# Kernel tuning notes

Hardware: AMD Instinct MI355X
Metric: run time of the kernel (lower is better)

## Reference

```python
import jax, jax.numpy as jnp
import numpy as np

N_NODES = 100000
N_EDGES = 1600000
N_PAIRS = 500000
IN_C, HID_C, OUT_C = 128, 128, 128


def setup_inputs() -> dict:
    key = jax.random.key(0)
    ks = jax.random.split(key, 12)
    def lin(k, fan_in, shape):
        b = 1.0 / np.sqrt(fan_in)
        return jax.random.uniform(k, shape, jnp.float32, -b, b)
    return {
        "x": jax.random.normal(ks[0], (N_NODES, IN_C), jnp.float32),
        "edge_index": jax.random.randint(ks[1], (2, N_EDGES), 0, N_NODES),
        "edge_pairs": jax.random.randint(ks[2], (2, N_PAIRS), 0, N_NODES),
        "W1": lin(ks[3], IN_C, (IN_C, HID_C)),
        "b1": jnp.zeros((HID_C,), jnp.float32),
        "W2": lin(ks[4], HID_C, (HID_C, OUT_C)),
        "b2": jnp.zeros((OUT_C,), jnp.float32),
        "Wm1": lin(ks[5], 2 * OUT_C, (2 * OUT_C, HID_C)),
        "bm1": lin(ks[6], 2 * OUT_C, (HID_C,)),
        "Wm2": lin(ks[7], HID_C, (HID_C, 1)),
        "bm2": lin(ks[8], HID_C, (1,)),
    }


def reference(x, edge_index, edge_pairs, W1, b1, W2, b2, Wm1, bm1, Wm2, bm2):
    N = x.shape[0]
    loop = jnp.arange(N, dtype=edge_index.dtype)
    row = jnp.concatenate([edge_index[0], loop])  # source nodes (+self loops)
    col = jnp.concatenate([edge_index[1], loop])  # target nodes (+self loops)
    # symmetric GCN normalization: deg^{-1/2}[row] * deg^{-1/2}[col]
    deg = jax.ops.segment_sum(jnp.ones(col.shape, x.dtype), col, num_segments=N)
    dinv = jnp.where(deg > 0, jax.lax.rsqrt(deg), 0.0)
    norm = dinv[row] * dinv[col]  # [E+N]

    def gcn_conv(h, W, b):
        h = h @ W  # transform first (PyG GCNConv lin has no bias)
        msg = h[row] * norm[:, None]
        return jax.ops.segment_sum(msg, col, num_segments=N) + b

    h = jax.nn.relu(gcn_conv(x, W1, b1))
    h = gcn_conv(h, W2, b2)  # dropout p=0.0 -> identity

    src, dst = edge_pairs[0], edge_pairs[1]
    ef = jnp.concatenate([h[src], h[dst]], axis=-1)  # [P, 2*out]
    out = jax.nn.relu(ef @ Wm1 + bm1) @ Wm2 + bm2
    return out.squeeze(-1)
```

## Files before the change

kernel.cpp:

```cpp
#include <hip/hip_runtime.h>
#include <hip/hip_fp16.h>

#define NCH 128
#define G_NODES 256
#define EPB 4096
#define RCAP 4864
#define MAXNB 512
#define KST 40

typedef __attribute__((ext_vector_type(8))) short short8;
typedef _Float16 half8 __attribute__((ext_vector_type(8)));
typedef __attribute__((ext_vector_type(4))) float floatx4;

static inline size_t align256(size_t x){ return (x + 255) & ~(size_t)255; }

__global__ __launch_bounds__(256) void binA_kernel(
    const int* __restrict__ row, const int* __restrict__ col,
    int* __restrict__ gcur, unsigned* __restrict__ bucketed, int E, int NB,
    const float* __restrict__ W1, const float* __restrict__ W2,
    const float* __restrict__ Wm1, short* __restrict__ planes){
  __shared__ int cnt[MAXNB];
  __shared__ int lbase[MAXNB];
  __shared__ int gbase[MAXNB];
  __shared__ unsigned sorted[EPB];
  __shared__ unsigned short binOf[EPB];
  __shared__ int sh[256];
  __shared__ int carry;
  int t = threadIdx.x;
  int e0 = blockIdx.x * EPB;
  int ecnt = min(EPB, E - e0);
  for (int i = t; i < NB; i += 256) cnt[i] = 0;
  if (t == 0) carry = 0;
  __syncthreads();
  unsigned rec[16]; int bn[16]; int rk[16];
  #pragma unroll
  for (int i = 0; i < 16; i++){
    int e = e0 + i * 256 + t;
    if (e < E){
      int r = row[e], c = col[e];
      bn[i]  = c >> 8;
      rec[i] = (unsigned)r | ((unsigned)(c & 255) << 17);
      rk[i]  = atomicAdd(&cnt[bn[i]], 1);
    } else bn[i] = -1;
  }
  __syncthreads();
  for (int start = 0; start < NB; start += 256){
    int i = start + t;
    int v = (i < NB) ? cnt[i] : 0;
    sh[t] = v; __syncthreads();
    for (int off = 1; off < 256; off <<= 1){
      int val = (t >= off) ? sh[t - off] : 0;
      __syncthreads(); sh[t] += val; __syncthreads();
    }
    if (i < NB) lbase[i] = sh[t] - v + carry;
    __syncthreads();
    if (t == 255) carry += sh[255];
    __syncthreads();
  }
  for (int i = t; i < NB; i += 256){
    int c = cnt[i];
    gbase[i] = (c > 0) ? atomicAdd(&gcur[i], c) : 0;
  }
  __syncthreads();
  #pragma unroll
  for (int i = 0; i < 16; i++){
    if (bn[i] >= 0){
      int pos = lbase[bn[i]] + rk[i];
      sorted[pos] = rec[i];
      binOf[pos]  = (unsigned short)bn[i];
    }
  }
  __syncthreads();
  for (int idx = t; idx < ecnt; idx += 256){
    int b = binOf[idx];
    int gpos = gbase[b] + (idx - lbase[b]);
    if (gpos < RCAP) bucketed[(size_t)b * RCAP + gpos] = sorted[idx];
  }
  {
    int gid = blockIdx.x * 256 + t;
    if (gid < 4 * 16384){
      int mat = gid >> 14;
      int idx = gid & 16383;
      int k = idx >> 7, n = idx & 127;
      const float* src = (mat == 0) ? W1 : (mat == 1) ? W2 : (mat == 2) ? Wm1 : (Wm1 + 16384);
      float x = src[idx];
      short hs, ls;
      if (mat == 0){
        unsigned u = __float_as_uint(x);
        hs = (short)(u >> 16);
        float hf = __uint_as_float(u & 0xFFFF0000u);
        ls = (short)(__float_as_uint(x - hf) >> 16);
      } else {
        __half h = __float2half(x);
        __half l = __float2half(x - __half2float(h));
        hs = __half_as_short(h); ls = __half_as_short(l);
      }
      planes[(size_t)(2 * mat) * 16384 + n * 128 + k]     = hs;
      planes[(size_t)(2 * mat + 1) * 16384 + n * 128 + k] = ls;
    }
  }
}

__global__ __launch_bounds__(512, 4) void fused_gemm_binB(
    const float* __restrict__ X, const short* __restrict__ Whi_,
    const short* __restrict__ Wlo_, __half* __restrict__ O, int nrows, int gemmBlocks,
    const unsigned* __restrict__ bucketed, const int* __restrict__ gcur,
    int* __restrict__ rows_sorted, int* __restrict__ offs,
    int* __restrict__ counts, float* __restrict__ dinv, int N){
  __shared__ __align__(16) char smem[40960];
  int t = threadIdx.x;
  if (blockIdx.x < gemmBlocks){
    short* Xhi = (short*)smem;
    short* Xlo = Xhi + 128 * KST;
    short* Whi = Xlo + 128 * KST;
    short* Wlo = Whi + 128 * KST;
    int w = t >> 6, lane = t & 63;
    int m = lane & 15, q = lane >> 4;
    int row0 = blockIdx.x * 128;
    floatx4 acc[8];
    #pragma unroll
    for (int ct = 0; ct < 8; ct++) acc[ct] = (floatx4)0.f;
    for (int kc = 0; kc < 4; kc++){
      int k0 = kc * 32;
      __syncthreads();
      #pragma unroll
      for (int qq = 0; qq < 2; qq++){
        int f = t + 512 * qq;
        int r = f >> 3, kq = f & 7;
        int gr = row0 + r;
        int grc = (gr < nrows) ? gr : 0;
        float4 v = *(const float4*)(X + (size_t)grc * NCH + k0 + kq * 4);
        short h[4], l[4];
        float vv[4] = {v.x, v.y, v.z, v.w};
        #pragma unroll
        for (int j = 0; j < 4; j++){
          unsigned u = __float_as_uint(vv[j]);
          h[j] = (short)(u >> 16);
          float hf = __uint_as_float(u & 0xFFFF0000u);
          l[j] = (short)(__float_as_uint(vv[j] - hf) >> 16);
        }
        *(uint2*)(Xhi + r * KST + kq * 4) = *(uint2*)h;
        *(uint2*)(Xlo + r * KST + kq * 4) = *(uint2*)l;
      }
      {
        int n = t >> 2, kq = t & 3;
        *(uint4*)(Whi + n * KST + kq * 8) = *(const uint4*)(Whi_ + n * NCH + k0 + kq * 8);
        *(uint4*)(Wlo + n * KST + kq * 8) = *(const uint4*)(Wlo_ + n * NCH + k0 + kq * 8);
      }
      __syncthreads();
      short8 a_hi = *(const short8*)(Xhi + (w * 16 + m) * KST + q * 8);
      short8 a_lo = *(const short8*)(Xlo + (w * 16 + m) * KST + q * 8);
      #pragma unroll
      for (int ct = 0; ct < 8; ct++){
        short8 b_hi = *(const short8*)(Whi + (ct * 16 + m) * KST + q * 8);
        short8 b_lo = *(const short8*)(Wlo + (ct * 16 + m) * KST + q * 8);
        acc[ct] = __builtin_amdgcn_mfma_f32_16x16x32_bf16(a_hi, b_hi, acc[ct], 0, 0, 0);
        acc[ct] = __builtin_amdgcn_mfma_f32_16x16x32_bf16(a_lo, b_hi, acc[ct], 0, 0, 0);
        acc[ct] = __builtin_amdgcn_mfma_f32_16x16x32_bf16(a_hi, b_lo, acc[ct], 0, 0, 0);
      }
    }
    #pragma unroll
    for (int r = 0; r < 4; r++){
      int grow = row0 + w * 16 + q * 4 + r;
      if (grow < nrows){
        #pragma unroll
        for (int ct = 0; ct < 8; ct++)
          O[(size_t)grow * NCH + ct * 16 + m] = __float2half(acc[ct][r]);
      }
    }
  } else {
    int b = blockIdx.x - gemmBlocks;
    unsigned* ledge = (unsigned*)smem;
    int* cnt  = (int*)(smem + RCAP * 4);
    int* cnt2 = cnt + 256;
    int* lex  = cnt2 + 256;
    int* sh   = lex + 256;
    int size = min(gcur[b], RCAP);
    int n0 = b * G_NODES;
    if (t < 256){ cnt[t] = 0; cnt2[t] = 0; }
    __syncthreads();
    for (int i = t; i < size; i += 512){
      unsigned v = bucketed[(size_t)b * RCAP + i];
      ledge[i] = v;
      atomicAdd(&cnt[v >> 17], 1);
    }
    __syncthreads();
    {
      int v = (t < 256) ? cnt[t] : 0;
      if (t < 256) sh[t] = v;
      __syncthreads();
      for (int off = 1; off < 256; off <<= 1){
        int val = (t >= off && t < 256) ? sh[t - off] : 0;
        __syncthreads();
        if (t < 256) sh[t] += val;
        __syncthreads();
      }
      if (t < 256){
        lex[t] = sh[t] - v;
        int n = n0 + t;
        if (n < N){
          counts[n] = v;
          offs[n]   = b * RCAP + sh[t] - v;
          dinv[n]   = rsqrtf((float)v + 1.0f);
        }
      }
    }
    __syncthreads();
    for (int i = t; i < size; i += 512){
      unsigned v = ledge[i];
      int node = v >> 17;
      int pos = lex[node] + atomicAdd(&cnt2[node], 1);
      rows_sorted[(size_t)b * RCAP + pos] = (int)(v & 0x1FFFFu);
    }
  }
}

template<int NCT>
__global__ __launch_bounds__(512, 4) void gemm_f16k(
    const __half* __restrict__ X,
    const short* __restrict__ Whi0, const short* __restrict__ Wlo0,
    const short* __restrict__ Whi1, const short* __restrict__ Wlo1,
    const float* __restrict__ scale, int do_scale,
    __half* __restrict__ O0, __half* __restrict__ O1, int nrows){
  __shared__ short Xs[128 * KST];
  __shared__ short Whs[NCT * 16 * KST];
  __shared__ short Wls[NCT * 16 * KST];
  int t = threadIdx.x;
  int w = t >> 6, lane = t & 63;
  int m = lane & 15, q = lane >> 4;
  int row0 = blockIdx.x * 128;
  floatx4 acc[NCT];
  #pragma unroll
  for (int ct = 0; ct < NCT; ct++) acc[ct] = (floatx4)0.f;

  for (int kc = 0; kc < 4; kc++){
    int k0 = kc * 32;
    __syncthreads();
    {
      int r = t >> 2, kq = t & 3;
      int gr = row0 + r;
      int grc = (gr < nrows) ? gr : 0;
      *(uint4*)(Xs + r * KST + kq * 8) = *(const uint4*)(X + (size_t)grc * NCH + k0 + kq * 8);
    }
    #pragma unroll
    for (int i = t; i < NCT * 16 * 4; i += 512){
      int n = i >> 2, kq = i & 3;
      const short* sh = (n < 128) ? (Whi0 + n * NCH) : (Whi1 + (n - 128) * NCH);
      const short* sl = (n < 128) ? (Wlo0 + n * NCH) : (Wlo1 + (n - 128) * NCH);
      *(uint4*)(Whs + n * KST + kq * 8) = *(const uint4*)(sh + k0 + kq * 8);
      *(uint4*)(Wls + n * KST + kq * 8) = *(const uint4*)(sl + k0 + kq * 8);
    }
    __syncthreads();
    half8 a = *(const half8*)(Xs + (w * 16 + m) * KST + q * 8);
    #pragma unroll
    for (int ct = 0; ct < NCT; ct++){
      half8 bh = *(const half8*)(Whs + (ct * 16 + m) * KST + q * 8);
      half8 bl = *(const half8*)(Wls + (ct * 16 + m) * KST + q * 8);
      acc[ct] = __builtin_amdgcn_mfma_f32_16x16x32_f16(a, bh, acc[ct], 0, 0, 0);
      acc[ct] = __builtin_amdgcn_mfma_f32_16x16x32_f16(a, bl, acc[ct], 0, 0, 0);
    }
  }
  #pragma unroll
  for (int r = 0; r < 4; r++){
    int grow = row0 + w * 16 + q * 4 + r;
    if (grow < nrows){
      float sc = do_scale ? scale[grow] : 1.0f;
      #pragma unroll
      for (int ct = 0; ct < NCT; ct++){
        __half val = __float2half(acc[ct][r] * sc);
        if (ct < 8) O0[(size_t)grow * NCH + ct * 16 + m] = val;
        else        O1[(size_t)grow * NCH + (ct - 8) * 16 + m] = val;
      }
    }
  }
}

__global__ __launch_bounds__(256) void agg_kernel(
    const __half* __restrict__ s, const float* __restrict__ dinv,
    const int* __restrict__ offs, const int* __restrict__ counts,
    const int* __restrict__ rows_sorted, const float* __restrict__ bias,
    __half* __restrict__ outp, int N, int do_relu, int edge_dinv){
  int wave = (int)((blockIdx.x * blockDim.x + threadIdx.x) >> 6);
  int lane = threadIdx.x & 63;
  if (wave >= N) return;
  int c = wave;
  int g = lane >> 4, h = lane & 15;
  float di = dinv[c];
  float wself = edge_dinv ? di : 1.0f;
  float acc[8] = {0.f,0.f,0.f,0.f,0.f,0.f,0.f,0.f};
  if (g == 0){
    uint4 v = *(const uint4*)(s + (size_t)c * NCH + h * 8);
    const __half2* hp = (const __half2*)&v;
    #pragma unroll
    for (int i = 0; i < 4; i++){
      float2 f = __half22float2(hp[i]);
      acc[2*i] = fmaf(wself, f.x, acc[2*i]); acc[2*i+1] = fmaf(wself, f.y, acc[2*i+1]);
    }
  }
  int off = offs[c], cnt = counts[c];
  for (int chunk = 0; chunk < cnt; chunk += 64){
    int nn = min(64, cnt - chunk);
    int myidx = (lane < nn) ? rows_sorted[off + chunk + lane] : 0;
    float mydinv = 1.0f;
    if (edge_dinv && lane < nn) mydinv = dinv[myidx];
    int jmax = (nn + 3) >> 2;
    #pragma unroll 8
    for (int j = 0; j < jmax; j++){
      int e = 4 * j + g;
      int r  = __shfl(myidx, e & 63, 64);
      float dr = edge_dinv ? __shfl(mydinv, e & 63, 64) : 1.0f;
      if (e < nn){
        uint4 v = *(const uint4*)(s + (size_t)r * NCH + h * 8);
        const __half2* hp = (const __half2*)&v;
        #pragma unroll
        for (int i = 0; i < 4; i++){
          float2 f = __half22float2(hp[i]);
          acc[2*i] = fmaf(dr, f.x, acc[2*i]); acc[2*i+1] = fmaf(dr, f.y, acc[2*i+1]);
        }
      }
    }
  }
  #pragma unroll
  for (int i = 0; i < 8; i++){
    acc[i] += __shfl_xor(acc[i], 16, 64);
    acc[i] += __shfl_xor(acc[i], 32, 64);
  }
  if (g == 0){
    float4 b0 = *(const float4*)(bias + h * 8);
    float4 b1 = *(const float4*)(bias + h * 8 + 4);
    float o[8];
    o[0] = di*acc[0]+b0.x; o[1] = di*acc[1]+b0.y; o[2] = di*acc[2]+b0.z; o[3] = di*acc[3]+b0.w;
    o[4] = di*acc[4]+b1.x; o[5] = di*acc[5]+b1.y; o[6] = di*acc[6]+b1.z; o[7] = di*acc[7]+b1.w;
    if (do_relu){
      #pragma unroll
      for (int i = 0; i < 8; i++) o[i] = fmaxf(o[i], 0.f);
    }
    __half2 packed[4];
    #pragma unroll
    for (int i = 0; i < 4; i++) packed[i] = __floats2half2_rn(o[2*i], o[2*i+1]);
    *(uint4*)(outp + (size_t)c * NCH + h * 8) = *(uint4*)packed;
  }
}

__global__ __launch_bounds__(256) void pair_kernel(
    const __half* __restrict__ A, const __half* __restrict__ B,
    const int* __restrict__ src, const int* __restrict__ dst,
    const float* __restrict__ bm1, const float* __restrict__ Wm2,
    const float* __restrict__ bm2, float* __restrict__ outp, int P){
  int gwave = (int)((blockIdx.x * blockDim.x + threadIdx.x) >> 6);
  int lane  = threadIdx.x & 63;
  int nw    = (int)((gridDim.x * blockDim.x) >> 6);
  int g = lane >> 4, h = lane & 15;
  float bb[8], ww[8];
  {
    float4 t0 = *(const float4*)(bm1 + h * 8);
    float4 t1 = *(const float4*)(bm1 + h * 8 + 4);
    bb[0]=t0.x; bb[1]=t0.y; bb[2]=t0.z; bb[3]=t0.w;
    bb[4]=t1.x; bb[5]=t1.y; bb[6]=t1.z; bb[7]=t1.w;
    float4 w0 = *(const float4*)(Wm2 + h * 8);
    float4 w1 = *(const float4*)(Wm2 + h * 8 + 4);
    ww[0]=w0.x; ww[1]=w0.y; ww[2]=w0.z; ww[3]=w0.w;
    ww[4]=w1.x; ww[5]=w1.y; ww[6]=w1.z; ww[7]=w1.w;
  }
  float bsc = bm2[0];
  const __half* basep = (g & 1) ? B : A;
  const int* idxp = (g & 1) ? dst : src;
  for (int p0 = gwave * 8; p0 < P; p0 += nw * 8){
    int piA = p0 + (g >> 1);
    int piB = p0 + 2 + (g >> 1);
    int piC = p0 + 4 + (g >> 1);
    int piD = p0 + 6 + (g >> 1);
    int piAX = (piA < P) ? piA : P - 1;
    int piBX = (piB < P) ? piB : P - 1;
    int piCX = (piC < P) ? piC : P - 1;
    int piDX = (piD < P) ? piD : P - 1;
    int nodeA = idxp[piAX];
    int nodeB = idxp[piBX];
    int nodeC = idxp[piCX];
    int nodeD = idxp[piDX];
    uint4 vA = *(const uint4*)(basep + (size_t)nodeA * NCH + h * 8);
    uint4 vB = *(const uint4*)(basep + (size_t)nodeB * NCH + h * 8);
    uint4 vC = *(const uint4*)(basep + (size_t)nodeC * NCH + h * 8);
    uint4 vD = *(const uint4*)(basep + (size_t)nodeD * NCH + h * 8);
    const __half2* hpA = (const __half2*)&vA;
    const __half2* hpB = (const __half2*)&vB;
    const __half2* hpC = (const __half2*)&vC;
    const __half2* hpD = (const __half2*)&vD;
    float fA[8], fB[8], fC[8], fD[8];
    #pragma unroll
    for (int i = 0; i < 4; i++){
      float2 ta = __half22float2(hpA[i]);
      float2 tb = __half22float2(hpB[i]);
      float2 tc = __half22float2(hpC[i]);
      float2 td = __half22float2(hpD[i]);
      fA[2*i] = ta.x; fA[2*i+1] = ta.y;
      fB[2*i] = tb.x; fB[2*i+1] = tb.y;
      fC[2*i] = tc.x; fC[2*i+1] = tc.y;
      fD[2*i] = td.x; fD[2*i+1] = td.y;
    }
    float pA = 0.f, pB = 0.f, pC = 0.f, pD = 0.f;
    #pragma unroll
    for (int i = 0; i < 8; i++){
      float oA = __shfl_xor(fA[i], 16, 64);
      float oB = __shfl_xor(fB[i], 16, 64);
      float oC = __shfl_xor(fC[i], 16, 64);
      float oD = __shfl_xor(fD[i], 16, 64);
      float zA = fmaxf(fA[i] + oA + bb[i], 0.f);
      float zB = fmaxf(fB[i] + oB + bb[i], 0.f);
      float zC = fmaxf(fC[i] + oC + bb[i], 0.f);
      float zD = fmaxf(fD[i] + oD + bb[i], 0.f);
      pA += zA * ww[i];
      pB += zB * ww[i];
      pC += zC * ww[i];
      pD += zD * ww[i];
    }
    #pragma unroll
    for (int d = 1; d <= 8; d <<= 1){
      pA += __shfl_xor(pA, d, 64);
      pB += __shfl_xor(pB, d, 64);
      pC += __shfl_xor(pC, d, 64);
      pD += __shfl_xor(pD, d, 64);
    }
    if ((lane & 31) == 0){
      if (piA < P) outp[piA] = pA + bsc;
      if (piB < P) outp[piB] = pB + bsc;
      if (piC < P) outp[piC] = pC + bsc;
      if (piD < P) outp[piD] = pD + bsc;
    }
  }
}


extern "C" void kernel_launch(void* const* d_in, const int* in_sizes, int n_in,
                              void* d_out, int out_size, void* d_ws, size_t ws_size,
                              hipStream_t stream){
  const float* x   = (const float*)d_in[0];
  const int*   ei  = (const int*)  d_in[1];
  const int*   ep  = (const int*)  d_in[2];
  const float* W1  = (const float*)d_in[3];
  const float* b1  = (const float*)d_in[4];
  const float* W2  = (const float*)d_in[5];
  const float* b2  = (const float*)d_in[6];
  const float* Wm1 = (const float*)d_in[7];
  const float* bm1 = (const float*)d_in[8];
  const float* Wm2 = (const float*)d_in[9];
  const float* bm2 = (const float*)d_in[10];
  float* outp = (float*)d_out;

  const int N = in_sizes[0] / NCH;
  const int E = in_sizes[1] / 2;
  const int P = in_sizes[2] / 2;
  const int NB = (N + G_NODES - 1) / G_NODES;

  char* base = (char*)d_ws;
  size_t off = 0;
  int*      counts      = (int*)     (base + off); off = align256(off + (size_t)N * 4);
  int*      offs        = (int*)     (base + off); off = align256(off + (size_t)N * 4);
  float*    dinv        = (float*)   (base + off); off = align256(off + (size_t)N * 4);
  int*      gcur        = (int*)     (base + off); off = align256(off + (size_t)NB * 4);
  unsigned* bucketed    = (unsigned*)(base + off); off = align256(off + (size_t)NB * RCAP * 4);
  int*      rows_sorted = (int*)     (base + off); off = align256(off + (size_t)NB * RCAP * 4);
  short*    planes      = (short*)   (base + off); off = align256(off + (size_t)8 * 16384 * 2);
  __half*   s1buf       = (__half*)  (base + off); off = align256(off + (size_t)N * NCH * 2);
  __half*   h1buf       = (__half*)  (base + off); off = align256(off + (size_t)N * NCH * 2);
  __half*   s2buf       = (__half*)  (base + off); off = align256(off + (size_t)N * NCH * 2);
  __half*   sA          = (__half*)  (base + off); off = align256(off + (size_t)N * NCH * 2);
  __half*   sB          = (__half*)  (base + off); off = align256(off + (size_t)N * NCH * 2);
  (void)ws_size; (void)n_in; (void)out_size;

  short* W1hi = planes + 0 * 16384;
  short* W1lo = planes + 1 * 16384;
  short* W2hi = planes + 2 * 16384;
  short* W2lo = planes + 3 * 16384;
  short* Wahi = planes + 4 * 16384;
  short* Walo = planes + 5 * 16384;
  short* Wbhi = planes + 6 * 16384;
  short* Wblo = planes + 7 * 16384;

  const int* row = ei;
  const int* col = ei + E;
  const int* psrc = ep;
  const int* pdst = ep + P;

  int gemm_grid = (N + 127) / 128;
  int agg_grid  = (N + 3) / 4;

  hipMemsetAsync(gcur, 0, (size_t)NB * 4, stream);
  binA_kernel<<<(E + EPB - 1) / EPB, 256, 0, stream>>>(row, col, gcur, bucketed, E, NB,
                                                       W1, W2, Wm1, planes);
  fused_gemm_binB<<<gemm_grid + NB, 512, 0, stream>>>(
      x, W1hi, W1lo, s1buf, N, gemm_grid,
      bucketed, gcur, rows_sorted, offs, counts, dinv, N);
  agg_kernel<<<agg_grid, 256, 0, stream>>>(s1buf, dinv, offs, counts, rows_sorted, b1, h1buf, N, 1, 1);
  gemm_f16k<8><<<gemm_grid, 512, 0, stream>>>(h1buf, W2hi, W2lo, W2hi, W2lo, dinv, 1, s2buf, s2buf, N);
  agg_kernel<<<agg_grid, 256, 0, stream>>>(s2buf, dinv, offs, counts, rows_sorted, b2, h1buf, N, 0, 0);
  gemm_f16k<16><<<gemm_grid, 512, 0, stream>>>(h1buf, Wahi, Walo, Wbhi, Wblo, dinv, 0, sA, sB, N);
  pair_kernel<<<8192, 256, 0, stream>>>(sA, sB, psrc, pdst, bm1, Wm2, bm2, outp, P);
}
```

Measured before the change: 377.1 us.

## Fold W2 into MLP weights to drop the second GCN GEMM

Uses linearity: the second GCN layer's transform W2 is precomputed into the MLP's first-layer weights (W2·Wm1 halves), and b2 is folded into the MLP bias. The second aggregation now runs directly on h1, and one full N×128×128 GEMM launch is removed. A small prep kernel computes the fused weight planes and bias. The fused weights are rounded to fp16 hi/lo, and the aggregation is applied before the transform, so rounding behaviour differs slightly.

```diff
diff --git a/kernel.cpp b/kernel.cpp
--- a/kernel.cpp
+++ b/kernel.cpp
@@ -14,11 +14,39 @@
 
 static inline size_t align256(size_t x){ return (x + 255) & ~(size_t)255; }
 
+__global__ __launch_bounds__(256) void wprep2_kernel(
+    const float* __restrict__ W2, const float* __restrict__ Wm1,
+    const float* __restrict__ b2, const float* __restrict__ bm1,
+    short* __restrict__ planes, float* __restrict__ bm1p, float* __restrict__ zbias){
+  int b = blockIdx.x, t = threadIdx.x;
+  if (b == 128){
+    if (t < 128){
+      float acc = bm1[t];
+      for (int j = 0; j < 128; j++)
+        acc += b2[j] * (Wm1[j * 128 + t] + Wm1[(128 + j) * 128 + t]);
+      bm1p[t] = acc;
+      zbias[t] = 0.f;
+    }
+    return;
+  }
+  __shared__ float w2row[128];
+  if (t < 128) w2row[t] = W2[b * 128 + t];
+  __syncthreads();
+  int mat = t >> 7, n = t & 127;
+  const float* Wsrc = Wm1 + (size_t)mat * 16384;
+  float acc = 0.f;
+  #pragma unroll 4
+  for (int j = 0; j < 128; j++) acc = fmaf(w2row[j], Wsrc[j * 128 + n], acc);
+  __half h = __float2half(acc);
+  __half l = __float2half(acc - __half2float(h));
+  planes[(size_t)(4 + 2 * mat) * 16384 + n * 128 + b] = __half_as_short(h);
+  planes[(size_t)(5 + 2 * mat) * 16384 + n * 128 + b] = __half_as_short(l);
+}
+
 __global__ __launch_bounds__(256) void binA_kernel(
     const int* __restrict__ row, const int* __restrict__ col,
     int* __restrict__ gcur, unsigned* __restrict__ bucketed, int E, int NB,
-    const float* __restrict__ W1, const float* __restrict__ W2,
-    const float* __restrict__ Wm1, short* __restrict__ planes){
+    const float* __restrict__ W1, short* __restrict__ planes){
   __shared__ int cnt[MAXNB];
   __shared__ int lbase[MAXNB];
   __shared__ int gbase[MAXNB];
@@ -78,25 +106,15 @@
   }
   {
     int gid = blockIdx.x * 256 + t;
-    if (gid < 4 * 16384){
-      int mat = gid >> 14;
-      int idx = gid & 16383;
-      int k = idx >> 7, n = idx & 127;
-      const float* src = (mat == 0) ? W1 : (mat == 1) ? W2 : (mat == 2) ? Wm1 : (Wm1 + 16384);
-      float x = src[idx];
-      short hs, ls;
-      if (mat == 0){
-        unsigned u = __float_as_uint(x);
-        hs = (short)(u >> 16);
-        float hf = __uint_as_float(u & 0xFFFF0000u);
-        ls = (short)(__float_as_uint(x - hf) >> 16);
-      } else {
-        __half h = __float2half(x);
-        __half l = __float2half(x - __half2float(h));
-        hs = __half_as_short(h); ls = __half_as_short(l);
-      }
-      planes[(size_t)(2 * mat) * 16384 + n * 128 + k]     = hs;
-      planes[(size_t)(2 * mat + 1) * 16384 + n * 128 + k] = ls;
+    if (gid < 16384){
+      int k = gid >> 7, n = gid & 127;
+      float x = W1[gid];
+      unsigned u = __float_as_uint(x);
+      short hs = (short)(u >> 16);
+      float hf = __uint_as_float(u & 0xFFFF0000u);
+      short ls = (short)(__float_as_uint(x - hf) >> 16);
+      planes[n * 128 + k]         = hs;
+      planes[16384 + n * 128 + k] = ls;
     }
   }
 }
@@ -461,17 +479,17 @@
   unsigned* bucketed    = (unsigned*)(base + off); off = align256(off + (size_t)NB * RCAP * 4);
   int*      rows_sorted = (int*)     (base + off); off = align256(off + (size_t)NB * RCAP * 4);
   short*    planes      = (short*)   (base + off); off = align256(off + (size_t)8 * 16384 * 2);
+  float*    bm1p        = (float*)   (base + off); off = align256(off + (size_t)256 * 4);
+  float*    zbias       = (float*)   (base + off); off = align256(off + (size_t)128 * 4);
   __half*   s1buf       = (__half*)  (base + off); off = align256(off + (size_t)N * NCH * 2);
   __half*   h1buf       = (__half*)  (base + off); off = align256(off + (size_t)N * NCH * 2);
-  __half*   s2buf       = (__half*)  (base + off); off = align256(off + (size_t)N * NCH * 2);
+  __half*   zbuf        = (__half*)  (base + off); off = align256(off + (size_t)N * NCH * 2);
   __half*   sA          = (__half*)  (base + off); off = align256(off + (size_t)N * NCH * 2);
   __half*   sB          = (__half*)  (base + off); off = align256(off + (size_t)N * NCH * 2);
   (void)ws_size; (void)n_in; (void)out_size;
 
   short* W1hi = planes + 0 * 16384;
   short* W1lo = planes + 1 * 16384;
-  short* W2hi = planes + 2 * 16384;
-  short* W2lo = planes + 3 * 16384;
   short* Wahi = planes + 4 * 16384;
   short* Walo = planes + 5 * 16384;
   short* Wbhi = planes + 6 * 16384;
@@ -485,15 +503,15 @@
   int gemm_grid = (N + 127) / 128;
   int agg_grid  = (N + 3) / 4;
 
+  wprep2_kernel<<<129, 256, 0, stream>>>(W2, Wm1, b2, bm1, planes, bm1p, zbias);
   hipMemsetAsync(gcur, 0, (size_t)NB * 4, stream);
   binA_kernel<<<(E + EPB - 1) / EPB, 256, 0, stream>>>(row, col, gcur, bucketed, E, NB,
-                                                       W1, W2, Wm1, planes);
+                                                       W1, planes);
   fused_gemm_binB<<<gemm_grid + NB, 512, 0, stream>>>(
       x, W1hi, W1lo, s1buf, N, gemm_grid,
       bucketed, gcur, rows_sorted, offs, counts, dinv, N);
   agg_kernel<<<agg_grid, 256, 0, stream>>>(s1buf, dinv, offs, counts, rows_sorted, b1, h1buf, N, 1, 1);
-  gemm_f16k<8><<<gemm_grid, 512, 0, stream>>>(h1buf, W2hi, W2lo, W2hi, W2lo, dinv, 1, s2buf, s2buf, N);
-  agg_kernel<<<agg_grid, 256, 0, stream>>>(s2buf, dinv, offs, counts, rows_sorted, b2, h1buf, N, 0, 0);
-  gemm_f16k<16><<<gemm_grid, 512, 0, stream>>>(h1buf, Wahi, Walo, Wbhi, Wblo, dinv, 0, sA, sB, N);
-  pair_kernel<<<8192, 256, 0, stream>>>(sA, sB, psrc, pdst, bm1, Wm2, bm2, outp, P);
-}
+  agg_kernel<<<agg_grid, 256, 0, stream>>>(h1buf, dinv, offs, counts, rows_sorted, zbias, zbuf, N, 0, 1);
+  gemm_f16k<16><<<gemm_grid, 512, 0, stream>>>(zbuf, Wahi, Walo, Wbhi, Wblo, dinv, 0, sA, sB, N);
+  pair_kernel<<<8192, 256, 0, stream>>>(sA, sB, psrc, pdst, bm1p, Wm2, bm2, outp, P);
+}
```

Result: no change. 374.9 us (-0.6%).
